# Performance work log

Hardware: AMD Instinct MI355X
Metric: run time of the kernel (lower is better)

The kernel has to match this reference:

```python
import jax, jax.numpy as jnp
import numpy as np
from jax import lax

B, NODE, T, D_IN = 8, 1024, 12, 16
HID, GAT_OUT, PRED_LEN = 32, 32, 6
HEADS = 3
F_IN = HID * T      # 384
C = GAT_OUT * T     # 384
N = B * NODE        # 8192
E = 65536


def setup_inputs() -> dict:
    key = jax.random.key(0)
    ks = jax.random.split(key, 24)
    s = 0.05
    inp = {}
    inp["x"] = jax.random.normal(ks[0], (B, NODE, T, D_IN), jnp.float32)
    inp["edge_index"] = jax.random.randint(ks[1], (2, E), 0, N)
    inp["edge_attr"] = jax.random.normal(ks[2], (E, 1), jnp.float32)
    inp["batch_vec"] = jnp.repeat(jnp.arange(B), NODE)
    inp["alpha"] = 1.0
    # GRU params (torch gate order: r, z, n)
    inp["Wih"] = jax.random.normal(ks[3], (3 * HID, D_IN), jnp.float32) * s
    inp["Whh"] = jax.random.normal(ks[4], (3 * HID, HID), jnp.float32) * s
    inp["bih"] = jax.random.normal(ks[5], (3 * HID,), jnp.float32) * s
    inp["bhh"] = jax.random.normal(ks[6], (3 * HID,), jnp.float32) * s
    # GATConv params
    inp["Wgat"] = jax.random.normal(ks[7], (HEADS * C, F_IN), jnp.float32) * s
    inp["att_src"] = jax.random.normal(ks[8], (1, HEADS, C), jnp.float32) * s
    inp["att_dst"] = jax.random.normal(ks[9], (1, HEADS, C), jnp.float32) * s
    inp["Wedge"] = jax.random.normal(ks[10], (HEADS * C, 1), jnp.float32) * s
    inp["att_edge"] = jax.random.normal(ks[11], (1, HEADS, C), jnp.float32) * s
    inp["gat_bias"] = jax.random.normal(ks[12], (C,), jnp.float32) * s
    # predictors / classifiers
    inp["Wp1"] = jax.random.normal(ks[13], (1, GAT_OUT), jnp.float32) * s
    inp["bp1"] = jax.random.normal(ks[14], (1,), jnp.float32) * s
    inp["Wp3"] = jax.random.normal(ks[15], (PRED_LEN, T), jnp.float32) * s
    inp["bp3"] = jax.random.normal(ks[16], (PRED_LEN,), jnp.float32) * s
    inp["Wc1"] = jax.random.normal(ks[17], (GAT_OUT, T * GAT_OUT), jnp.float32) * s
    inp["bc1"] = jax.random.normal(ks[18], (GAT_OUT,), jnp.float32) * s
    inp["Wc2"] = jax.random.normal(ks[19], (2, GAT_OUT), jnp.float32) * s
    inp["bc2"] = jax.random.normal(ks[20], (2,), jnp.float32) * s
    return inp


def _gru(x, Wih, Whh, bih, bhh):
    # x: [rows, T, D_IN] -> [rows, T, HID]
    h0 = jnp.zeros((x.shape[0], HID), x.dtype)

    def step(h, xt):
        gi = xt @ Wih.T + bih
        gh = h @ Whh.T + bhh
        ir, iz, inn = jnp.split(gi, 3, axis=-1)
        hr, hz, hn = jnp.split(gh, 3, axis=-1)
        r = jax.nn.sigmoid(ir + hr)
        z = jax.nn.sigmoid(iz + hz)
        n = jnp.tanh(inn + r * hn)
        h_new = (1.0 - z) * n + z * h
        return h_new, h_new

    _, hs = lax.scan(step, h0, jnp.swapaxes(x, 0, 1))
    return jnp.swapaxes(hs, 0, 1)


def _gat(x, edge_index, edge_attr, Wgat, att_src, att_dst, Wedge, att_edge, bias):
    # PyG GATConv, heads=HEADS, concat=False, edge_dim=1, no self loops
    h = (x @ Wgat.T).reshape(N, HEADS, C)          # [N,H,C]
    a_src = (h * att_src).sum(-1)                  # [N,H]
    a_dst = (h * att_dst).sum(-1)                  # [N,H]
    src, dst = edge_index[0], edge_index[1]
    e = (edge_attr @ Wedge.T).reshape(-1, HEADS, C)
    a_edge = (e * att_edge).sum(-1)                # [E,H]
    a = jax.nn.leaky_relu(a_src[src] + a_dst[dst] + a_edge, 0.2)
    amax = jax.ops.segment_max(a, dst, num_segments=N)
    a = jnp.exp(a - amax[dst])
    denom = jax.ops.segment_sum(a, dst, num_segments=N)
    a = a / (denom[dst] + 1e-16)                   # segment softmax over incoming edges
    msg = h[src] * a[:, :, None]                   # [E,H,C]
    out = jax.ops.segment_sum(msg, dst, num_segments=N)
    return out.mean(axis=1) + bias                 # concat=False -> head mean


def reference(x, edge_index, edge_attr, batch_vec, alpha,
              Wih, Whh, bih, bhh,
              Wgat, att_src, att_dst, Wedge, att_edge, gat_bias,
              Wp1, bp1, Wp3, bp3, Wc1, bc1, Wc2, bc2):
    gru_in = x.reshape(-1, T, D_IN)                       # [N,T,D]
    gru_out = _gru(gru_in, Wih, Whh, bih, bhh)            # [N,T,HID]
    gat_in = gru_out.reshape(N, F_IN)
    gat_out = _gat(gat_in, edge_index, edge_attr, Wgat, att_src, att_dst,
                   Wedge, att_edge, gat_bias)             # [N,C]
    lin_in = gat_out.reshape(-1, T, GAT_OUT)              # [N,T,GAT_OUT]
    p = jax.nn.relu(jnp.einsum('ntc,oc->nto', lin_in, Wp1) + bp1).squeeze(-1)  # [N,T]
    p = jax.nn.relu(p @ Wp3.T + bp3)                      # [N,PRED_LEN]
    out_pred = p.reshape(B, NODE, PRED_LEN)
    # GRL is identity in forward
    pooled = jax.ops.segment_max(gat_out, batch_vec, num_segments=B)  # [B,C]
    l1 = pooled @ Wc1.T + bc1
    l2 = l1 @ Wc2.T + bc2
    out_label = jax.nn.softmax(l2, axis=1)
    return out_pred, out_label
```

## Files before the change

kernel.cpp:

```cpp
#include <hip/hip_runtime.h>
#include <hip/hip_bf16.h>

#define N_NODES 8192
#define E_EDGES 65536
#define HEADS 3
#define CDIM 384
#define NHC 1152
#define T_STEPS 12
#define D_IN 16
#define HID 32
#define PRED_LEN 6
#define OUT_LABEL_OFF 49152

#define O_X        0u
#define O_WIH      1572864u
#define O_WHH      1574400u
#define O_BIH      1577472u
#define O_BHH      1577568u
#define O_WGAT     1577664u
#define O_ATTS     2020032u
#define O_ATTD     2021184u
#define O_WEDGE    2022336u
#define O_ATTE     2023488u
#define O_GBIAS    2024640u
#define O_WP1      2025024u
#define O_BP1      2025056u
#define O_WP3      2025057u
#define O_BP3      2025129u
#define O_WC1      2025135u
#define O_BC1      2037423u
#define O_WC2      2037455u
#define O_BC2      2037519u
#define O_EATTR    2037521u
#define CONV_TOTAL 2103057u

#define O_GATIN    2103072u
#define O_GATB     O_GATIN
#define O_WGATB    (O_GATIN + 1572864u)
#define O_DEG      (O_GATIN + 1794048u)
#define O_ROWST    (O_GATIN + 1802240u)
#define O_CURS     (O_GATIN + 1810432u)
#define O_CSRE     (O_GATIN + 1818624u)
#define O_HFEAT    5248800u
#define O_ASRC     14685984u
#define O_ADST     14710560u
#define O_ARAW     14735136u
#define O_WEXP     14931744u
#define O_AMAX     15128352u
#define O_DENOM    15152928u
#define O_GMEAN    15177504u
#define O_POOLED   18323232u
#define O_KH       18326304u
#define O_FLAG     18326307u

typedef __attribute__((ext_vector_type(8))) short short8;
typedef __attribute__((ext_vector_type(4))) float floatx4;

__device__ __forceinline__ float b2f(unsigned short u) {
    return __uint_as_float(((unsigned)u) << 16);
}
__device__ __forceinline__ unsigned short f2b(float f) {
    __hip_bfloat16 b = __float2bfloat16(f);
    return *(unsigned short*)&b;
}
__device__ __forceinline__ unsigned enc_f(float f) {
    unsigned u = __float_as_uint(f);
    return (u & 0x80000000u) ? ~u : (u | 0x80000000u);
}
__device__ __forceinline__ float dec_f(unsigned e) {
    return __uint_as_float((e & 0x80000000u) ? (e & 0x7FFFFFFFu) : ~e);
}

__global__ void detect_kernel(const unsigned short* __restrict__ wih_raw,
                              int* __restrict__ flag)
{
    int lane = threadIdx.x;
    int cnt = 0;
#pragma unroll
    for (int i = 0; i < 8; i++) {
        unsigned short h = wih_raw[(lane * 8 + i) * 2];
        int e = (h >> 7) & 0xFF;
        if (e >= 100 && e <= 127) cnt++;
    }
#pragma unroll
    for (int off = 32; off; off >>= 1) cnt += __shfl_down(cnt, off, 64);
    if (lane == 0) *flag = (cnt >= 300) ? 1 : 0;
}

__global__ __launch_bounds__(256) void convert_all(
    const int* __restrict__ flag,
    const void* x, const void* Wih, const void* Whh, const void* bih, const void* bhh,
    const void* Wgat, const void* atts, const void* attd, const void* Wedge, const void* atte,
    const void* gbias, const void* Wp1, const void* bp1, const void* Wp3, const void* bp3,
    const void* Wc1, const void* bc1, const void* Wc2, const void* bc2, const void* eattr,
    float* __restrict__ dst)
{
    unsigned idx = blockIdx.x * 256 + threadIdx.x;
    if (idx >= CONV_TOTAL) return;
    const void* src; unsigned off;
    if      (idx < O_WIH)   { src = x;     off = idx - O_X; }
    else if (idx < O_WHH)   { src = Wih;   off = idx - O_WIH; }
    else if (idx < O_BIH)   { src = Whh;   off = idx - O_WHH; }
    else if (idx < O_BHH)   { src = bih;   off = idx - O_BIH; }
    else if (idx < O_WGAT)  { src = bhh;   off = idx - O_BHH; }
    else if (idx < O_ATTS)  { src = Wgat;  off = idx - O_WGAT; }
    else if (idx < O_ATTD)  { src = atts;  off = idx - O_ATTS; }
    else if (idx < O_WEDGE) { src = attd;  off = idx - O_ATTD; }
    else if (idx < O_ATTE)  { src = Wedge; off = idx - O_WEDGE; }
    else if (idx < O_GBIAS) { src = atte;  off = idx - O_ATTE; }
    else if (idx < O_WP1)   { src = gbias; off = idx - O_GBIAS; }
    else if (idx < O_BP1)   { src = Wp1;   off = idx - O_WP1; }
    else if (idx < O_BP3)   { src = (idx < O_BP1 + 1) ? bp1 : Wp3; off = (idx < O_BP1 + 1) ? 0 : idx - O_BP3 + 72; }
    else if (idx < O_WC1)   { src = bp3;   off = idx - O_BP3; }
    else if (idx < O_BC1)   { src = Wc1;   off = idx - O_WC1; }
    else if (idx < O_WC2)   { src = bc1;   off = idx - O_BC1; }
    else if (idx < O_BC2)   { src = Wc2;   off = idx - O_WC2; }
    else if (idx < O_EATTR) { src = bc2;   off = idx - O_BC2; }
    else                    { src = eattr; off = idx - O_EATTR; }
    if (idx >= O_BP1 && idx < O_BP3) {
        if (idx == O_BP1) { src = bp1; off = 0; }
        else              { src = Wp3; off = idx - O_WP3; }
    }
    float v = (*flag) ? b2f(((const unsigned short*)src)[off])
                      : ((const float*)src)[off];
    dst[idx] = v;
}

__global__ void cvt_wgat(const int* __restrict__ flag,
                         const void* __restrict__ Wg,
                         unsigned short* __restrict__ dstb)
{
    unsigned i = blockIdx.x * 256 + threadIdx.x;
    if (i >= 442368u) return;
    dstb[i] = (*flag) ? ((const unsigned short*)Wg)[i]
                      : f2b(((const float*)Wg)[i]);
}

__global__ __launch_bounds__(256) void gru_kernel(
    const float* __restrict__ xf,
    const float* __restrict__ Wih,
    const float* __restrict__ Whh,
    const float* __restrict__ bih,
    const float* __restrict__ bhh,
    unsigned short* __restrict__ gat_b)
{
    __shared__ float hsh[8][32];
    int gid = blockIdx.x * 256 + threadIdx.x;
    int n = gid >> 5;
    int j = gid & 31;
    int wid = threadIdx.x >> 5;

    float wih[3][16], whh[3][32], bi[3], bh[3];
#pragma unroll
    for (int g = 0; g < 3; g++) {
        int row = g * 32 + j;
#pragma unroll
        for (int i = 0; i < 16; i++) wih[g][i] = Wih[row * 16 + i];
#pragma unroll
        for (int i = 0; i < 32; i++) whh[g][i] = Whh[row * 32 + i];
        bi[g] = bih[row];
        bh[g] = bhh[row];
    }

    float hval = 0.f;
    hsh[wid][j] = 0.f;

    const float4* x4 = (const float4*)(xf + (size_t)n * 192);

    for (int t = 0; t < T_STEPS; t++) {
        float xv[16];
#pragma unroll
        for (int q = 0; q < 4; q++) {
            float4 p = x4[t * 4 + q];
            xv[q * 4 + 0] = p.x; xv[q * 4 + 1] = p.y;
            xv[q * 4 + 2] = p.z; xv[q * 4 + 3] = p.w;
        }

        float ir = bi[0], iz = bi[1], in_ = bi[2];
#pragma unroll
        for (int i = 0; i < 16; i++) {
            ir  += wih[0][i] * xv[i];
            iz  += wih[1][i] * xv[i];
            in_ += wih[2][i] * xv[i];
        }
        float hr = bh[0], hz = bh[1], hn = bh[2];
#pragma unroll
        for (int q = 0; q < 8; q++) {
            float4 hv = *(const float4*)&hsh[wid][q * 4];
            hr += whh[0][q*4+0]*hv.x + whh[0][q*4+1]*hv.y + whh[0][q*4+2]*hv.z + whh[0][q*4+3]*hv.w;
            hz += whh[1][q*4+0]*hv.x + whh[1][q*4+1]*hv.y + whh[1][q*4+2]*hv.z + whh[1][q*4+3]*hv.w;
            hn += whh[2][q*4+0]*hv.x + whh[2][q*4+1]*hv.y + whh[2][q*4+2]*hv.z + whh[2][q*4+3]*hv.w;
        }
        float r = 1.f / (1.f + expf(-(ir + hr)));
        float z = 1.f / (1.f + expf(-(iz + hz)));
        float nn = tanhf(in_ + r * hn);
        hval = (1.f - z) * nn + z * hval;

        gat_b[(size_t)n * 384 + t * 32 + j] = f2b(hval);
        hsh[wid][j] = hval;
    }
}

__global__ __launch_bounds__(256) void gemm_mfma(
    const unsigned short* __restrict__ Ab,
    const unsigned short* __restrict__ Bb,
    unsigned short* __restrict__ Cb)
{
    __shared__ unsigned short sA[128][40];
    __shared__ unsigned short sB[128][40];
    int tid = threadIdx.x;
    int wave = tid >> 6, lane = tid & 63;
    int wm = (wave >> 1) * 64, wn = (wave & 1) * 64;
    int m0 = blockIdx.x * 128, n0 = blockIdx.y * 128;

    int r0 = tid >> 2;
    int c8 = (tid & 3) * 8;

    floatx4 acc[4][4];
#pragma unroll
    for (int i = 0; i < 4; i++)
#pragma unroll
        for (int j = 0; j < 4; j++) acc[i][j] = 0;

    int ml = lane & 15, kq = (lane >> 4) * 8;

    for (int k0 = 0; k0 < 384; k0 += 32) {
        short8 a0 = *(const short8*)(Ab + (size_t)(m0 + r0) * 384 + k0 + c8);
        short8 a1 = *(const short8*)(Ab + (size_t)(m0 + r0 + 64) * 384 + k0 + c8);
        short8 b0 = *(const short8*)(Bb + (size_t)(n0 + r0) * 384 + k0 + c8);
        short8 b1 = *(const short8*)(Bb + (size_t)(n0 + r0 + 64) * 384 + k0 + c8);

        __syncthreads();
        *(short8*)(&sA[r0][c8])      = a0;
        *(short8*)(&sA[r0 + 64][c8]) = a1;
        *(short8*)(&sB[r0][c8])      = b0;
        *(short8*)(&sB[r0 + 64][c8]) = b1;
        __syncthreads();

        short8 af[4], bf[4];
#pragma unroll
        for (int i = 0; i < 4; i++)
            af[i] = *(const short8*)(&sA[wm + i * 16 + ml][kq]);
#pragma unroll
        for (int j = 0; j < 4; j++)
            bf[j] = *(const short8*)(&sB[wn + j * 16 + ml][kq]);
#pragma unroll
        for (int i = 0; i < 4; i++)
#pragma unroll
            for (int j = 0; j < 4; j++)
                acc[i][j] = __builtin_amdgcn_mfma_f32_16x16x32_bf16(af[i], bf[j], acc[i][j], 0, 0, 0);
    }

    int cn = lane & 15, rq = (lane >> 4) * 4;
#pragma unroll
    for (int i = 0; i < 4; i++)
#pragma unroll
        for (int j = 0; j < 4; j++)
#pragma unroll
            for (int r = 0; r < 4; r++)
                Cb[(size_t)(m0 + wm + i * 16 + rq + r) * NHC + n0 + wn + j * 16 + cn] = f2b(acc[i][j][r]);
}

__global__ __launch_bounds__(256) void att_score_kernel(
    const unsigned short* __restrict__ h_bf,
    const float* __restrict__ att_src,
    const float* __restrict__ att_dst,
    float* __restrict__ a_src, float* __restrict__ a_dst)
{
    int w = (blockIdx.x * 256 + threadIdx.x) >> 6;
    int lane = threadIdx.x & 63;
    int n = w / 3, hd = w % 3;
    const unsigned short* hrow = h_bf + (size_t)n * NHC + hd * CDIM;
    float s0 = 0.f, s1 = 0.f;
#pragma unroll
    for (int q = 0; q < 6; q++) {
        int c = lane + q * 64;
        float hv = b2f(hrow[c]);
        s0 += hv * att_src[hd * CDIM + c];
        s1 += hv * att_dst[hd * CDIM + c];
    }
#pragma unroll
    for (int off = 32; off; off >>= 1) {
        s0 += __shfl_down(s0, off, 64);
        s1 += __shfl_down(s1, off, 64);
    }
    if (lane == 0) { a_src[n * 3 + hd] = s0; a_dst[n * 3 + hd] = s1; }
}

__global__ void edge_const_kernel(const float* __restrict__ Wedge,
                                  const float* __restrict__ att_edge,
                                  float* __restrict__ Kh)
{
    int hd = threadIdx.x >> 6, lane = threadIdx.x & 63;
    float s = 0.f;
#pragma unroll
    for (int q = 0; q < 6; q++) {
        int c = lane + q * 64;
        s += Wedge[hd * CDIM + c] * att_edge[hd * CDIM + c];
    }
#pragma unroll
    for (int off = 32; off; off >>= 1) s += __shfl_down(s, off, 64);
    if (lane == 0) Kh[hd] = s;
}

__global__ __launch_bounds__(256) void edge_score_kernel(
    const int* __restrict__ edge_index,
    const float* __restrict__ edge_attr,
    const float* __restrict__ a_src, const float* __restrict__ a_dst,
    const float* __restrict__ Kh,
    float* __restrict__ a_raw, unsigned* __restrict__ amax_enc,
    int* __restrict__ deg)
{
    int tid = blockIdx.x * 256 + threadIdx.x;
    int hd = tid >> 16;
    int e = tid & (E_EDGES - 1);
    int src = edge_index[e];
    int dst = edge_index[E_EDGES + e];
    float a = a_src[src * 3 + hd] + a_dst[dst * 3 + hd] + edge_attr[e] * Kh[hd];
    a = a > 0.f ? a : 0.2f * a;
    a_raw[hd * E_EDGES + e] = a;
    atomicMax(&amax_enc[dst * 3 + hd], enc_f(a));
    if (hd == 0) atomicAdd(&deg[dst], 1);
}

__global__ __launch_bounds__(256) void scan_kernel(
    const int* __restrict__ deg, int* __restrict__ rowstart, int* __restrict__ cursor)
{
    __shared__ int ps[256];
    int t = threadIdx.x;
    int l[32], s = 0;
#pragma unroll
    for (int i = 0; i < 32; i++) { l[i] = deg[t * 32 + i]; s += l[i]; }
    ps[t] = s;
    __syncthreads();
    if (t == 0) {
        int run = 0;
        for (int i = 0; i < 256; i++) { int v = ps[i]; ps[i] = run; run += v; }
    }
    __syncthreads();
    int b = ps[t];
#pragma unroll
    for (int i = 0; i < 32; i++) {
        rowstart[t * 32 + i] = b;
        cursor[t * 32 + i] = b;
        b += l[i];
    }
}

__global__ __launch_bounds__(256) void edge_exp_kernel(
    const int* __restrict__ edge_index,
    const float* __restrict__ a_raw, const unsigned* __restrict__ amax_enc,
    float* __restrict__ w_exp, float* __restrict__ denom,
    int* __restrict__ cursor, int* __restrict__ csr_e)
{
    int tid = blockIdx.x * 256 + threadIdx.x;
    int hd = tid >> 16;
    int e = tid & (E_EDGES - 1);
    int dst = edge_index[E_EDGES + e];
    float m = dec_f(amax_enc[dst * 3 + hd]);
    float w = expf(a_raw[hd * E_EDGES + e] - m);
    w_exp[hd * E_EDGES + e] = w;
    unsafeAtomicAdd(&denom[dst * 3 + hd], w);
    if (hd == 0) {
        int pos = atomicAdd(&cursor[dst], 1);
        csr_e[pos] = e;
    }
}

__global__ __launch_bounds__(384) void aggregate_fused(
    const int* __restrict__ flag,
    const int* __restrict__ edge_index,
    const unsigned short* __restrict__ h_bf,
    const float* __restrict__ w_exp, const float* __restrict__ denom,
    const int* __restrict__ rowstart, const int* __restrict__ deg,
    const int* __restrict__ csr_e,
    const float* __restrict__ gat_bias,
    const float* __restrict__ Wp1, const float* __restrict__ bp1,
    const float* __restrict__ Wp3, const float* __restrict__ bp3,
    float* __restrict__ gmean,
    void* __restrict__ out_pred)
{
    int dst = blockIdx.x;
    int s = rowstart[dst], d = deg[dst];
    int tid = threadIdx.x;
    const float third = 1.f / 3.f;
    float inv0 = third / (denom[dst * 3 + 0] + 1e-16f);
    float inv1 = third / (denom[dst * 3 + 1] + 1e-16f);
    float inv2 = third / (denom[dst * 3 + 2] + 1e-16f);
    __shared__ int ssrc[64];
    __shared__ float sc0[64], sc1[64], sc2[64];
    __shared__ float gs[384];
    __shared__ float ps[12];
    float a = 0.f;
    for (int ch = 0; ch < d; ch += 64) {
        int m = d - ch; if (m > 64) m = 64;
        __syncthreads();
        if (tid < m) {
            int e = csr_e[s + ch + tid];
            ssrc[tid] = edge_index[e];
            sc0[tid] = w_exp[e] * inv0;
            sc1[tid] = w_exp[E_EDGES + e] * inv1;
            sc2[tid] = w_exp[2 * E_EDGES + e] * inv2;
        }
        __syncthreads();
        for (int i = 0; i < m; i++) {
            const unsigned short* hs = h_bf + (size_t)ssrc[i] * NHC;
            a += sc0[i] * b2f(hs[tid]) + sc1[i] * b2f(hs[tid + CDIM]) + sc2[i] * b2f(hs[tid + 2 * CDIM]);
        }
    }
    float g = a + gat_bias[tid];
    gmean[(size_t)dst * CDIM + tid] = g;
    gs[tid] = g;
    __syncthreads();

    int t = tid >> 5, c = tid & 31;
    float v = gs[t * 32 + c] * Wp1[c];
#pragma unroll
    for (int off = 16; off; off >>= 1) v += __shfl_down(v, off, 32);
    if (c == 0) { float p = v + bp1[0]; ps[t] = p > 0.f ? p : 0.f; }
    __syncthreads();

    if (tid < PRED_LEN) {
        float acc = bp3[tid];
#pragma unroll
        for (int tt = 0; tt < 12; tt++) acc += Wp3[tid * 12 + tt] * ps[tt];
        acc = acc > 0.f ? acc : 0.f;
        size_t oi = (size_t)dst * PRED_LEN + tid;
        if (*flag) ((__hip_bfloat16*)out_pred)[oi] = __float2bfloat16(acc);
        else       ((float*)out_pred)[oi] = acc;
    }
}

__global__ __launch_bounds__(384) void pool_kernel(
    const float* __restrict__ gmean,
    unsigned* __restrict__ pooled_enc)
{
    int b = blockIdx.x, ch = blockIdx.y;
    int tid = threadIdx.x;
    const float* base = gmean + ((size_t)b * 1024 + ch * 64) * CDIM + tid;
    float m = -3.4e38f;
    for (int i = 0; i < 64; i++)
        m = fmaxf(m, base[(size_t)i * CDIM]);
    atomicMax(&pooled_enc[b * CDIM + tid], enc_f(m));
}

__global__ __launch_bounds__(256) void cls_kernel(
    const int* __restrict__ flag,
    const unsigned* __restrict__ pooled_enc,
    const float* __restrict__ Wc1, const float* __restrict__ bc1,
    const float* __restrict__ Wc2, const float* __restrict__ bc2,
    void* __restrict__ out_base)
{
    __shared__ float l1s[8][32];
    int b = threadIdx.x >> 5, i = threadIdx.x & 31;
    float acc = bc1[i];
    for (int c = 0; c < CDIM; c++)
        acc += Wc1[i * CDIM + c] * dec_f(pooled_enc[b * CDIM + c]);
    l1s[b][i] = acc;
    __syncthreads();
    if (threadIdx.x < 8) {
        int bb = threadIdx.x;
        float l0 = bc2[0], l1v = bc2[1];
#pragma unroll
        for (int ii = 0; ii < 32; ii++) {
            l0  += Wc2[ii] * l1s[bb][ii];
            l1v += Wc2[32 + ii] * l1s[bb][ii];
        }
        float m = fmaxf(l0, l1v);
        float e0 = expf(l0 - m), e1 = expf(l1v - m);
        float s = e0 + e1;
        if (*flag) {
            __hip_bfloat16* ob = (__hip_bfloat16*)out_base;
            ob[OUT_LABEL_OFF + bb * 2 + 0] = __float2bfloat16(e0 / s);
            ob[OUT_LABEL_OFF + bb * 2 + 1] = __float2bfloat16(e1 / s);
        } else {
            float* of = (float*)out_base;
            of[OUT_LABEL_OFF + bb * 2 + 0] = e0 / s;
            of[OUT_LABEL_OFF + bb * 2 + 1] = e1 / s;
        }
    }
}

extern "C" void kernel_launch(void* const* d_in, const int* in_sizes, int n_in,
                              void* d_out, int out_size, void* d_ws, size_t ws_size,
                              hipStream_t stream) {
    float* W = (float*)d_ws;
    int* flag = (int*)(W + O_FLAG);
    const int* edge_index = (const int*)d_in[1];

    size_t zero_floats = (size_t)(O_POOLED + 8 * CDIM) - O_AMAX;
    hipMemsetAsync(W + O_AMAX, 0, zero_floats * 4, stream);
    hipMemsetAsync(W + O_DEG, 0, 8192 * 4, stream);

    detect_kernel<<<1, 64, 0, stream>>>((const unsigned short*)d_in[5], flag);
    convert_all<<<(CONV_TOTAL + 255) / 256, 256, 0, stream>>>(
        flag,
        d_in[0], d_in[5], d_in[6], d_in[7], d_in[8],
        d_in[9], d_in[10], d_in[11], d_in[12], d_in[13],
        d_in[14], d_in[15], d_in[16], d_in[17], d_in[18],
        d_in[19], d_in[20], d_in[21], d_in[22], d_in[2],
        W);
    cvt_wgat<<<(442368 + 255) / 256, 256, 0, stream>>>(
        flag, d_in[9], (unsigned short*)(W + O_WGATB));

    gru_kernel<<<N_NODES * 32 / 256, 256, 0, stream>>>(
        W + O_X, W + O_WIH, W + O_WHH, W + O_BIH, W + O_BHH,
        (unsigned short*)(W + O_GATB));
    gemm_mfma<<<dim3(N_NODES / 128, NHC / 128), 256, 0, stream>>>(
        (const unsigned short*)(W + O_GATB),
        (const unsigned short*)(W + O_WGATB),
        (unsigned short*)(W + O_HFEAT));
    att_score_kernel<<<(N_NODES * 3 * 64) / 256, 256, 0, stream>>>(
        (const unsigned short*)(W + O_HFEAT), W + O_ATTS, W + O_ATTD,
        W + O_ASRC, W + O_ADST);
    edge_const_kernel<<<1, 192, 0, stream>>>(W + O_WEDGE, W + O_ATTE, W + O_KH);
    edge_score_kernel<<<3 * E_EDGES / 256, 256, 0, stream>>>(
        edge_index, W + O_EATTR, W + O_ASRC, W + O_ADST, W + O_KH,
        W + O_ARAW, (unsigned*)(W + O_AMAX), (int*)(W + O_DEG));
    scan_kernel<<<1, 256, 0, stream>>>(
        (const int*)(W + O_DEG), (int*)(W + O_ROWST), (int*)(W + O_CURS));
    edge_exp_kernel<<<3 * E_EDGES / 256, 256, 0, stream>>>(
        edge_index, W + O_ARAW, (const unsigned*)(W + O_AMAX),
        W + O_WEXP, W + O_DENOM, (int*)(W + O_CURS), (int*)(W + O_CSRE));
    aggregate_fused<<<N_NODES, 384, 0, stream>>>(
        flag, edge_index, (const unsigned short*)(W + O_HFEAT),
        W + O_WEXP, W + O_DENOM,
        (const int*)(W + O_ROWST), (const int*)(W + O_DEG),
        (const int*)(W + O_CSRE),
        W + O_GBIAS, W + O_WP1, W + O_BP1, W + O_WP3, W + O_BP3,
        W + O_GMEAN, d_out);
    pool_kernel<<<dim3(8, 16), 384, 0, stream>>>(
        W + O_GMEAN, (unsigned*)(W + O_POOLED));
    cls_kernel<<<1, 256, 0, stream>>>(
        flag, (const unsigned*)(W + O_POOLED),
        W + O_WC1, W + O_BC1, W + O_WC2, W + O_BC2, d_out);
}
```

Baseline: 284.5 us.

## Merge small kernels and memsets, parallelize scan and classifier head

```diff
diff --git a/kernel.cpp b/kernel.cpp
--- a/kernel.cpp
+++ b/kernel.cpp
@@ -71,20 +71,29 @@
     return __uint_as_float((e & 0x80000000u) ? (e & 0x7FFFFFFFu) : ~e);
 }
 
-__global__ void detect_kernel(const unsigned short* __restrict__ wih_raw,
-                              int* __restrict__ flag)
-{
-    int lane = threadIdx.x;
-    int cnt = 0;
-#pragma unroll
-    for (int i = 0; i < 8; i++) {
-        unsigned short h = wih_raw[(lane * 8 + i) * 2];
-        int e = (h >> 7) & 0xFF;
-        if (e >= 100 && e <= 127) cnt++;
-    }
-#pragma unroll
-    for (int off = 32; off; off >>= 1) cnt += __shfl_down(cnt, off, 64);
-    if (lane == 0) *flag = (cnt >= 300) ? 1 : 0;
+__global__ __launch_bounds__(256) void fill_detect(
+    const unsigned short* __restrict__ wih_raw,
+    int* __restrict__ flag,
+    float* __restrict__ W)
+{
+    if (blockIdx.x == 0 && threadIdx.x < 64) {
+        int lane = threadIdx.x;
+        int cnt = 0;
+#pragma unroll
+        for (int i = 0; i < 8; i++) {
+            unsigned short h = wih_raw[(lane * 8 + i) * 2];
+            int e = (h >> 7) & 0xFF;
+            if (e >= 100 && e <= 127) cnt++;
+        }
+#pragma unroll
+        for (int off = 32; off; off >>= 1) cnt += __shfl_down(cnt, off, 64);
+        if (lane == 0) *flag = (cnt >= 300) ? 1 : 0;
+    }
+    unsigned idx = blockIdx.x * 256 + threadIdx.x;
+    if      (idx < 24576u) W[O_AMAX  + idx] = 0.f;
+    else if (idx < 49152u) W[O_DENOM + idx - 24576u] = 0.f;
+    else if (idx < 52224u) W[O_POOLED + idx - 49152u] = 0.f;
+    else if (idx < 60416u) ((int*)(W + O_DEG))[idx - 52224u] = 0;
 }
 
 __global__ __launch_bounds__(256) void convert_all(
@@ -93,50 +102,41 @@
     const void* Wgat, const void* atts, const void* attd, const void* Wedge, const void* atte,
     const void* gbias, const void* Wp1, const void* bp1, const void* Wp3, const void* bp3,
     const void* Wc1, const void* bc1, const void* Wc2, const void* bc2, const void* eattr,
-    float* __restrict__ dst)
+    float* __restrict__ dst, unsigned short* __restrict__ wgatb)
 {
     unsigned idx = blockIdx.x * 256 + threadIdx.x;
     if (idx >= CONV_TOTAL) return;
+    if (idx >= O_WGAT && idx < O_ATTS) {
+        unsigned off = idx - O_WGAT;
+        wgatb[off] = (*flag) ? ((const unsigned short*)Wgat)[off]
+                             : f2b(((const float*)Wgat)[off]);
+        return;
+    }
     const void* src; unsigned off;
     if      (idx < O_WIH)   { src = x;     off = idx - O_X; }
     else if (idx < O_WHH)   { src = Wih;   off = idx - O_WIH; }
     else if (idx < O_BIH)   { src = Whh;   off = idx - O_WHH; }
     else if (idx < O_BHH)   { src = bih;   off = idx - O_BIH; }
     else if (idx < O_WGAT)  { src = bhh;   off = idx - O_BHH; }
-    else if (idx < O_ATTS)  { src = Wgat;  off = idx - O_WGAT; }
     else if (idx < O_ATTD)  { src = atts;  off = idx - O_ATTS; }
     else if (idx < O_WEDGE) { src = attd;  off = idx - O_ATTD; }
     else if (idx < O_ATTE)  { src = Wedge; off = idx - O_WEDGE; }
     else if (idx < O_GBIAS) { src = atte;  off = idx - O_ATTE; }
     else if (idx < O_WP1)   { src = gbias; off = idx - O_GBIAS; }
     else if (idx < O_BP1)   { src = Wp1;   off = idx - O_WP1; }
-    else if (idx < O_BP3)   { src = (idx < O_BP1 + 1) ? bp1 : Wp3; off = (idx < O_BP1 + 1) ? 0 : idx - O_BP3 + 72; }
+    else if (idx < O_BP3)   { src = (idx == O_BP1) ? bp1 : Wp3; off = (idx == O_BP1) ? 0 : idx - O_WP3; }
     else if (idx < O_WC1)   { src = bp3;   off = idx - O_BP3; }
     else if (idx < O_BC1)   { src = Wc1;   off = idx - O_WC1; }
     else if (idx < O_WC2)   { src = bc1;   off = idx - O_BC1; }
     else if (idx < O_BC2)   { src = Wc2;   off = idx - O_WC2; }
     else if (idx < O_EATTR) { src = bc2;   off = idx - O_BC2; }
     else                    { src = eattr; off = idx - O_EATTR; }
-    if (idx >= O_BP1 && idx < O_BP3) {
-        if (idx == O_BP1) { src = bp1; off = 0; }
-        else              { src = Wp3; off = idx - O_WP3; }
-    }
     float v = (*flag) ? b2f(((const unsigned short*)src)[off])
                       : ((const float*)src)[off];
     dst[idx] = v;
 }
 
-__global__ void cvt_wgat(const int* __restrict__ flag,
-                         const void* __restrict__ Wg,
-                         unsigned short* __restrict__ dstb)
-{
-    unsigned i = blockIdx.x * 256 + threadIdx.x;
-    if (i >= 442368u) return;
-    dstb[i] = (*flag) ? ((const unsigned short*)Wg)[i]
-                      : f2b(((const float*)Wg)[i]);
-}
-
-__global__ __launch_bounds__(256) void gru_kernel(
+__global__ __launch_bounds__(256, 2) void gru_kernel(
     const float* __restrict__ xf,
     const float* __restrict__ Wih,
     const float* __restrict__ Whh,
@@ -176,12 +176,12 @@
             xv[q * 4 + 2] = p.z; xv[q * 4 + 3] = p.w;
         }
 
-        float ir = bi[0], iz = bi[1], in_ = bi[2];
+        float ir = bi[0], iz = bi[1], inn = bi[2];
 #pragma unroll
         for (int i = 0; i < 16; i++) {
             ir  += wih[0][i] * xv[i];
             iz  += wih[1][i] * xv[i];
-            in_ += wih[2][i] * xv[i];
+            inn += wih[2][i] * xv[i];
         }
         float hr = bh[0], hz = bh[1], hn = bh[2];
 #pragma unroll
@@ -193,7 +193,7 @@
         }
         float r = 1.f / (1.f + expf(-(ir + hr)));
         float z = 1.f / (1.f + expf(-(iz + hz)));
-        float nn = tanhf(in_ + r * hn);
+        float nn = tanhf(inn + r * hn);
         hval = (1.f - z) * nn + z * hval;
 
         gat_b[(size_t)n * 384 + t * 32 + j] = f2b(hval);
@@ -265,8 +265,26 @@
     const unsigned short* __restrict__ h_bf,
     const float* __restrict__ att_src,
     const float* __restrict__ att_dst,
-    float* __restrict__ a_src, float* __restrict__ a_dst)
-{
+    const float* __restrict__ Wedge,
+    const float* __restrict__ att_edge,
+    float* __restrict__ a_src, float* __restrict__ a_dst,
+    float* __restrict__ Kh)
+{
+    if (blockIdx.x == (N_NODES * 3) / 4) {
+        if (threadIdx.x < 192) {
+            int hd = threadIdx.x >> 6, lane = threadIdx.x & 63;
+            float s = 0.f;
+#pragma unroll
+            for (int q = 0; q < 6; q++) {
+                int c = lane + q * 64;
+                s += Wedge[hd * CDIM + c] * att_edge[hd * CDIM + c];
+            }
+#pragma unroll
+            for (int off = 32; off; off >>= 1) s += __shfl_down(s, off, 64);
+            if (lane == 0) Kh[hd] = s;
+        }
+        return;
+    }
     int w = (blockIdx.x * 256 + threadIdx.x) >> 6;
     int lane = threadIdx.x & 63;
     int n = w / 3, hd = w % 3;
@@ -285,22 +303,6 @@
         s1 += __shfl_down(s1, off, 64);
     }
     if (lane == 0) { a_src[n * 3 + hd] = s0; a_dst[n * 3 + hd] = s1; }
-}
-
-__global__ void edge_const_kernel(const float* __restrict__ Wedge,
-                                  const float* __restrict__ att_edge,
-                                  float* __restrict__ Kh)
-{
-    int hd = threadIdx.x >> 6, lane = threadIdx.x & 63;
-    float s = 0.f;
-#pragma unroll
-    for (int q = 0; q < 6; q++) {
-        int c = lane + q * 64;
-        s += Wedge[hd * CDIM + c] * att_edge[hd * CDIM + c];
-    }
-#pragma unroll
-    for (int off = 32; off; off >>= 1) s += __shfl_down(s, off, 64);
-    if (lane == 0) Kh[hd] = s;
 }
 
 __global__ __launch_bounds__(256) void edge_score_kernel(
@@ -326,19 +328,24 @@
 __global__ __launch_bounds__(256) void scan_kernel(
     const int* __restrict__ deg, int* __restrict__ rowstart, int* __restrict__ cursor)
 {
-    __shared__ int ps[256];
+    __shared__ int wtot[4];
     int t = threadIdx.x;
+    int lane = t & 63, wv = t >> 6;
     int l[32], s = 0;
 #pragma unroll
     for (int i = 0; i < 32; i++) { l[i] = deg[t * 32 + i]; s += l[i]; }
-    ps[t] = s;
+    int sc = s;
+#pragma unroll
+    for (int off = 1; off <= 32; off <<= 1) {
+        int v = __shfl_up(sc, off, 64);
+        if (lane >= off) sc += v;
+    }
+    if (lane == 63) wtot[wv] = sc;
     __syncthreads();
-    if (t == 0) {
-        int run = 0;
-        for (int i = 0; i < 256; i++) { int v = ps[i]; ps[i] = run; run += v; }
-    }
-    __syncthreads();
-    int b = ps[t];
+    int woff = 0;
+#pragma unroll
+    for (int w = 0; w < 4; w++) if (w < wv) woff += wtot[w];
+    int b = woff + sc - s;
 #pragma unroll
     for (int i = 0; i < 32; i++) {
         rowstart[t * 32 + i] = b;
@@ -444,39 +451,44 @@
     atomicMax(&pooled_enc[b * CDIM + tid], enc_f(m));
 }
 
-__global__ __launch_bounds__(256) void cls_kernel(
+__global__ __launch_bounds__(384) void cls_kernel(
     const int* __restrict__ flag,
     const unsigned* __restrict__ pooled_enc,
     const float* __restrict__ Wc1, const float* __restrict__ bc1,
     const float* __restrict__ Wc2, const float* __restrict__ bc2,
     void* __restrict__ out_base)
 {
-    __shared__ float l1s[8][32];
-    int b = threadIdx.x >> 5, i = threadIdx.x & 31;
-    float acc = bc1[i];
-    for (int c = 0; c < CDIM; c++)
-        acc += Wc1[i * CDIM + c] * dec_f(pooled_enc[b * CDIM + c]);
-    l1s[b][i] = acc;
+    int b = blockIdx.x, t = threadIdx.x;
+    __shared__ float l1[32];
+    if (t < 32) l1[t] = bc1[t];
     __syncthreads();
-    if (threadIdx.x < 8) {
-        int bb = threadIdx.x;
+    float v = dec_f(pooled_enc[b * CDIM + t]);
+#pragma unroll
+    for (int i = 0; i < 32; i++) {
+        float p = v * Wc1[i * CDIM + t];
+#pragma unroll
+        for (int off = 32; off; off >>= 1) p += __shfl_down(p, off, 64);
+        if ((t & 63) == 0) atomicAdd(&l1[i], p);
+    }
+    __syncthreads();
+    if (t == 0) {
         float l0 = bc2[0], l1v = bc2[1];
 #pragma unroll
         for (int ii = 0; ii < 32; ii++) {
-            l0  += Wc2[ii] * l1s[bb][ii];
-            l1v += Wc2[32 + ii] * l1s[bb][ii];
+            l0  += Wc2[ii] * l1[ii];
+            l1v += Wc2[32 + ii] * l1[ii];
         }
         float m = fmaxf(l0, l1v);
         float e0 = expf(l0 - m), e1 = expf(l1v - m);
         float s = e0 + e1;
         if (*flag) {
             __hip_bfloat16* ob = (__hip_bfloat16*)out_base;
-            ob[OUT_LABEL_OFF + bb * 2 + 0] = __float2bfloat16(e0 / s);
-            ob[OUT_LABEL_OFF + bb * 2 + 1] = __float2bfloat16(e1 / s);
+            ob[OUT_LABEL_OFF + b * 2 + 0] = __float2bfloat16(e0 / s);
+            ob[OUT_LABEL_OFF + b * 2 + 1] = __float2bfloat16(e1 / s);
         } else {
             float* of = (float*)out_base;
-            of[OUT_LABEL_OFF + bb * 2 + 0] = e0 / s;
-            of[OUT_LABEL_OFF + bb * 2 + 1] = e1 / s;
+            of[OUT_LABEL_OFF + b * 2 + 0] = e0 / s;
+            of[OUT_LABEL_OFF + b * 2 + 1] = e1 / s;
         }
     }
 }
@@ -488,20 +500,15 @@
     int* flag = (int*)(W + O_FLAG);
     const int* edge_index = (const int*)d_in[1];
 
-    size_t zero_floats = (size_t)(O_POOLED + 8 * CDIM) - O_AMAX;
-    hipMemsetAsync(W + O_AMAX, 0, zero_floats * 4, stream);
-    hipMemsetAsync(W + O_DEG, 0, 8192 * 4, stream);
-
-    detect_kernel<<<1, 64, 0, stream>>>((const unsigned short*)d_in[5], flag);
+    fill_detect<<<236, 256, 0, stream>>>(
+        (const unsigned short*)d_in[5], flag, W);
     convert_all<<<(CONV_TOTAL + 255) / 256, 256, 0, stream>>>(
         flag,
         d_in[0], d_in[5], d_in[6], d_in[7], d_in[8],
         d_in[9], d_in[10], d_in[11], d_in[12], d_in[13],
         d_in[14], d_in[15], d_in[16], d_in[17], d_in[18],
         d_in[19], d_in[20], d_in[21], d_in[22], d_in[2],
-        W);
-    cvt_wgat<<<(442368 + 255) / 256, 256, 0, stream>>>(
-        flag, d_in[9], (unsigned short*)(W + O_WGATB));
+        W, (unsigned short*)(W + O_WGATB));
 
     gru_kernel<<<N_NODES * 32 / 256, 256, 0, stream>>>(
         W + O_X, W + O_WIH, W + O_WHH, W + O_BIH, W + O_BHH,
@@ -510,10 +517,10 @@
         (const unsigned short*)(W + O_GATB),
         (const unsigned short*)(W + O_WGATB),
         (unsigned short*)(W + O_HFEAT));
-    att_score_kernel<<<(N_NODES * 3 * 64) / 256, 256, 0, stream>>>(
+    att_score_kernel<<<(N_NODES * 3) / 4 + 1, 256, 0, stream>>>(
         (const unsigned short*)(W + O_HFEAT), W + O_ATTS, W + O_ATTD,
-        W + O_ASRC, W + O_ADST);
-    edge_const_kernel<<<1, 192, 0, stream>>>(W + O_WEDGE, W + O_ATTE, W + O_KH);
+        W + O_WEDGE, W + O_ATTE,
+        W + O_ASRC, W + O_ADST, W + O_KH);
     edge_score_kernel<<<3 * E_EDGES / 256, 256, 0, stream>>>(
         edge_index, W + O_EATTR, W + O_ASRC, W + O_ADST, W + O_KH,
         W + O_ARAW, (unsigned*)(W + O_AMAX), (int*)(W + O_DEG));
@@ -531,7 +538,7 @@
         W + O_GMEAN, d_out);
     pool_kernel<<<dim3(8, 16), 384, 0, stream>>>(
         W + O_GMEAN, (unsigned*)(W + O_POOLED));
-    cls_kernel<<<1, 256, 0, stream>>>(
+    cls_kernel<<<8, 384, 0, stream>>>(
         flag, (const unsigned*)(W + O_POOLED),
         W + O_WC1, W + O_BC1, W + O_WC2, W + O_BC2, d_out);
 }
```

Measured after the change: 274.1 us. 1.04x faster.
